# Performance work log

Hardware: AMD Instinct MI355X
Metric: run time of the kernel (lower is better)

Reference implementation:

```python
import jax, jax.numpy as jnp
import numpy as np

MEM_SIZE = 1_000_000
DIM = 128
BS = 256
K = 1024
TEMP = 0.07
MOM_V = 0.5
MOM_A = 0.5


def _l2norm(x, axis=-1, eps=1e-12):
    n = jnp.sqrt(jnp.sum(x * x, axis=axis, keepdims=True))
    return x / jnp.maximum(n, eps)


def setup_inputs() -> dict:
    key = jax.random.key(0)
    k1, k2, k3, k4, k5, k6 = jax.random.split(key, 6)
    video_emb = jax.random.normal(k1, (BS, DIM), dtype=jnp.float32)
    audio_emb = jax.random.normal(k2, (BS, DIM), dtype=jnp.float32)
    y = jax.random.randint(k3, (BS,), 0, MEM_SIZE, dtype=jnp.int32)
    # alias method draws over memory_size-1 items (before shifting past y)
    neg_idx = jax.random.randint(k4, (BS, K), 0, MEM_SIZE - 1, dtype=jnp.int32)
    view1_mem = _l2norm(jax.random.normal(k5, (MEM_SIZE, DIM), dtype=jnp.float32))
    view2_mem = _l2norm(jax.random.normal(k6, (MEM_SIZE, DIM), dtype=jnp.float32))
    return {
        "video_emb": video_emb,
        "audio_emb": audio_emb,
        "y": y,
        "neg_idx": neg_idx,
        "view1_mem": view1_mem,
        "view2_mem": view2_mem,
    }


def reference(video_emb, audio_emb, y, neg_idx, view1_mem, view2_mem):
    v = _l2norm(video_emb, axis=1)   # [bs, dim]
    a = _l2norm(audio_emb, axis=1)   # [bs, dim]

    # shift negative indices past the positive index y (as in sample_negatives)
    idx = neg_idx + (neg_idx >= y[:, None]).astype(neg_idx.dtype)  # [bs, K]

    # gather positives / negatives from memory banks
    v_pos = view1_mem[y]           # [bs, dim]
    a_pos = view2_mem[y]           # [bs, dim]
    v_neg = view1_mem[idx]         # [bs, K, dim]
    a_neg = view2_mem[idx]         # [bs, K, dim]

    # xModal scores (wModal=False)
    v2a_pos = jnp.einsum("bd,bd->b", a_pos, v)[:, None] / TEMP    # [bs, 1]
    v2a_neg = jnp.einsum("bkd,bd->bk", a_neg, v) / TEMP           # [bs, K]
    a2v_pos = jnp.einsum("bd,bd->b", v_pos, a)[:, None] / TEMP    # [bs, 1]
    a2v_neg = jnp.einsum("bkd,bd->bk", v_neg, a) / TEMP           # [bs, K]

    scores = jnp.stack(
        [jnp.concatenate([v2a_pos, v2a_neg], axis=1),
         jnp.concatenate([a2v_pos, a2v_neg], axis=1)],
        axis=0,
    )  # [2, bs, K+1]

    # momentum scatter update of memory banks (no_grad in original)
    new1 = _l2norm(MOM_V * v_pos + (1.0 - MOM_V) * v, axis=1)
    new2 = _l2norm(MOM_A * a_pos + (1.0 - MOM_A) * a, axis=1)
    view1_new = view1_mem.at[y].set(new1)
    view2_new = view2_mem.at[y].set(new2)

    return scores, view1_new, view2_new
```

## Files before the change

### kernel.cpp

```cpp
#include <hip/hip_runtime.h>

#define MEM_SIZE 1000000
#define DIM 128
#define BS 256
#define K 1024
#define NSC (K + 1)
#define OVFCAP 32768

constexpr float INV_TEMP = 1.0f / 0.07f;
constexpr float MOM = 0.5f;

#define NB 2048
#define BT 128
#define NWAVES (NB * BT / 64)

typedef float fx4 __attribute__((ext_vector_type(4)));

#define QTAB_OFF 0
#define CNT_OFF  262144
#define SLOT_OFF 4456448
#define OVFC_OFF 12845056
#define OVF_OFF  12845312
#define WS_NEED  13107456

__device__ __forceinline__ float wave_reduce_sum(float v) {
    #pragma unroll
    for (int off = 32; off > 0; off >>= 1)
        v += __shfl_xor(v, off, 64);
    return v;
}

__global__ __launch_bounds__(BT) void setup_kernel(
    const float* __restrict__ video, const float* __restrict__ audio,
    float* __restrict__ qtab, int* __restrict__ counts,
    int* __restrict__ slots_i, int* __restrict__ ovf_cnt) {
    const int bid = blockIdx.x;
    const int t = threadIdx.x;
    const int tid = bid * BT + t;
    if (bid < 256) {
        const int u = bid * 2 + (t >> 6);
        const int lane = t & 63;
        const int b = u & (BS - 1);
        const float* src = (u < BS) ? video : audio;
        const float2 e = reinterpret_cast<const float2*>(src + b * DIM)[lane];
        const float ss = wave_reduce_sum(e.x * e.x + e.y * e.y);
        const float inv = 1.0f / fmaxf(sqrtf(ss), 1e-12f);
        reinterpret_cast<float2*>(qtab + u * DIM)[lane] =
            make_float2(e.x * inv, e.y * inv);
    }
    for (int i = tid; i < MEM_SIZE; i += NB * BT) counts[i] = 0;
    for (int i = tid; i < 2 * MEM_SIZE; i += NB * BT) slots_i[i] = -1;
    if (tid == 0) *ovf_cnt = 0;
}

__global__ void build_kernel(const int* __restrict__ y,
                             const int* __restrict__ neg,
                             int* __restrict__ counts,
                             int* __restrict__ slots_i,
                             int* __restrict__ ovf_cnt,
                             int2* __restrict__ ovf) {
    const int E = blockIdx.x * blockDim.x + threadIdx.x;
    int b, j, row;
    if (E < BS * K) {
        b = E >> 10;
        const int jj = E & 1023;
        j = jj + 1;
        const int ni = neg[b * K + jj];
        const int yb = y[b];
        row = ni + (ni >= yb ? 1 : 0);
    } else {
        b = E - BS * K;
        if (b >= BS) return;
        j = 0;
        row = y[b];
    }
    const int key = (b << 11) | j;
    const int old = atomicAdd(&counts[row], 1);
    if (old < 2) {
        slots_i[row * 2 + old] = key;
    } else {
        const int p = atomicAdd(ovf_cnt, 1);
        if (p < OVFCAP) ovf[p] = make_int2(row, key);
    }
}

__global__ __launch_bounds__(BT, 4) void main_kernel(
    const float* __restrict__ view1, const float* __restrict__ view2,
    const float* __restrict__ qtab, const int2* __restrict__ slots,
    float* __restrict__ scores,
    fx4* __restrict__ out1, fx4* __restrict__ out2) {
    const int tid = blockIdx.x * BT + threadIdx.x;
    const int wid = tid >> 6;
    const int lane = tid & 63;
    const int half = lane >> 5;
    const int hl = lane & 31;
    const fx4* s1 = reinterpret_cast<const fx4*>(view1);
    const fx4* s2 = reinterpret_cast<const fx4*>(view2);
    const fx4* qt4 = reinterpret_cast<const fx4*>(qtab);

    const long long n4 = (long long)MEM_SIZE * DIM / 4;
    for (long long wbase = (long long)wid * 64; wbase < n4;
         wbase += (long long)NWAVES * 64) {
        const long long i = wbase + lane;
        const fx4 a = s1[i];
        const fx4 c = s2[i];
        const int row = (int)(wbase >> 5) + half;
        const int2 sl = slots[row];
        __builtin_nontemporal_store(a, &out1[i]);
        __builtin_nontemporal_store(c, &out2[i]);

        if (__any(sl.x >= 0)) {
            #pragma unroll
            for (int t = 0; t < 2; ++t) {
                const int key = (t == 0) ? sl.x : sl.y;
                if (key >= 0) {
                    const int b = key >> 11;
                    const int j = key & 2047;
                    const fx4 q0 = qt4[b * 32 + hl];
                    const fx4 q1 = qt4[(256 + b) * 32 + hl];
                    float d0 = q0.x * c.x + q0.y * c.y + q0.z * c.z + q0.w * c.w;
                    float d1 = q1.x * a.x + q1.y * a.y + q1.z * a.z + q1.w * a.w;
                    #pragma unroll
                    for (int off = 16; off > 0; off >>= 1) {
                        d0 += __shfl_xor(d0, off, 64);
                        d1 += __shfl_xor(d1, off, 64);
                    }
                    if (hl == 0) {
                        scores[b * NSC + j] = d0 * INV_TEMP;
                        scores[(256 + b) * NSC + j] = d1 * INV_TEMP;
                    }
                }
            }
        }
    }
}

__global__ void tail_kernel(const float* __restrict__ video,
                            const float* __restrict__ audio,
                            const int* __restrict__ y,
                            const float* __restrict__ view1,
                            const float* __restrict__ view2,
                            const float* __restrict__ qtab,
                            const int* __restrict__ ovf_cnt,
                            const int2* __restrict__ ovf,
                            float* __restrict__ scores,
                            float* __restrict__ out1,
                            float* __restrict__ out2) {
    const int blk = blockIdx.x;
    const int lane = threadIdx.x;
    if (blk < 512) {
        const int bank = blk >> 8;
        const int b = blk & (BS - 1);
        const int row = y[b];
        for (int b2 = b + 1; b2 < BS; ++b2)
            if (y[b2] == row) return;
        const float* emb = (bank == 0) ? video : audio;
        const float2 e = reinterpret_cast<const float2*>(emb + b * DIM)[lane];
        const float ss = wave_reduce_sum(e.x * e.x + e.y * e.y);
        const float inv = 1.0f / fmaxf(sqrtf(ss), 1e-12f);
        const float* mem = (bank == 0) ? view1 : view2;
        const float2 xp =
            reinterpret_cast<const float2*>(mem + (size_t)row * DIM)[lane];
        float2 nv = make_float2(MOM * xp.x + (1.0f - MOM) * e.x * inv,
                                MOM * xp.y + (1.0f - MOM) * e.y * inv);
        const float ss2 = wave_reduce_sum(nv.x * nv.x + nv.y * nv.y);
        const float inv2 = 1.0f / fmaxf(sqrtf(ss2), 1e-12f);
        float* out = (bank == 0) ? out1 : out2;
        reinterpret_cast<float2*>(out + (size_t)row * DIM)[lane] =
            make_float2(nv.x * inv2, nv.y * inv2);
    } else {
        int n = *ovf_cnt;
        if (n > OVFCAP) n = OVFCAP;
        const float2* m1 = reinterpret_cast<const float2*>(view1);
        const float2* m2 = reinterpret_cast<const float2*>(view2);
        const float2* qt2 = reinterpret_cast<const float2*>(qtab);
        for (int e = blk - 512; e < n; e += 128) {
            const int2 rk = ovf[e];
            const int row = rk.x, key = rk.y;
            const int b = key >> 11, j = key & 2047;
            const float2 xa = m1[(size_t)row * 64 + lane];
            const float2 xc = m2[(size_t)row * 64 + lane];
            const float2 q0 = qt2[(size_t)b * 64 + lane];
            const float2 q1 = qt2[(size_t)(256 + b) * 64 + lane];
            float d0 = xc.x * q0.x + xc.y * q0.y;
            float d1 = xa.x * q1.x + xa.y * q1.y;
            #pragma unroll
            for (int off = 32; off > 0; off >>= 1) {
                d0 += __shfl_xor(d0, off, 64);
                d1 += __shfl_xor(d1, off, 64);
            }
            if (lane == 0) {
                scores[b * NSC + j] = d0 * INV_TEMP;
                scores[(256 + b) * NSC + j] = d1 * INV_TEMP;
            }
        }
    }
}

__global__ __launch_bounds__(256) void fb_fused(
    const float* __restrict__ video, const float* __restrict__ audio,
    const int* __restrict__ y, const int* __restrict__ neg,
    const float* __restrict__ view1, const float* __restrict__ view2,
    float* __restrict__ scores,
    fx4* __restrict__ out1, fx4* __restrict__ out2) {
    const int bid = blockIdx.x;
    const int tid = threadIdx.x;
    if ((bid & 3) == 0) {
        const int bm = bid >> 2;
        const int m = bm >> 8;
        const int b = bm & (BS - 1);
        const int lane = tid & 63;
        const int wv = tid >> 6;
        const int yb = y[b];
        const float* emb = (m == 0) ? video : audio;
        const float2 e = reinterpret_cast<const float2*>(emb + b * DIM)[lane];
        const float ss = wave_reduce_sum(e.x * e.x + e.y * e.y);
        const float inv = 1.0f / fmaxf(sqrtf(ss), 1e-12f);
        const float vx = e.x * inv, vy = e.y * inv;
        const float2* mem2 =
            reinterpret_cast<const float2*>((m == 0) ? view2 : view1);
        float* srow = scores + (size_t)bm * NSC;
        const int* nb = neg + b * K;
        const int chunk = (NSC + 3) / 4;
        const int j0 = wv * chunk;
        const int j1 = min(NSC, j0 + chunk);
        for (int j = j0; j < j1; ++j) {
            int r0;
            if (j == 0) r0 = yb;
            else { const int ni = nb[j - 1]; r0 = ni + (ni >= yb ? 1 : 0); }
            const float2 x0 = mem2[(size_t)r0 * 64 + lane];
            const float s0 = wave_reduce_sum(x0.x * vx + x0.y * vy);
            if (lane == 0) srow[j] = s0 * INV_TEMP;
        }
    } else {
        const long long n4 = (long long)MEM_SIZE * DIM / 4;
        const int cb = bid - (bid >> 2) - 1;
        const fx4* s1 = reinterpret_cast<const fx4*>(view1);
        const fx4* s2 = reinterpret_cast<const fx4*>(view2);
        long long i = (long long)cb * blockDim.x + tid;
        const long long stride = (long long)1536 * blockDim.x;
        for (; i < n4; i += stride) {
            const fx4 a = __builtin_nontemporal_load(&s1[i]);
            const fx4 c = __builtin_nontemporal_load(&s2[i]);
            __builtin_nontemporal_store(a, &out1[i]);
            __builtin_nontemporal_store(c, &out2[i]);
        }
    }
}

__global__ void fb_scatter(const float* __restrict__ video,
                           const float* __restrict__ audio,
                           const int* __restrict__ y,
                           const float* __restrict__ view1,
                           const float* __restrict__ view2,
                           float* __restrict__ out1,
                           float* __restrict__ out2) {
    const int blk = blockIdx.x;
    const int lane = threadIdx.x;
    const int bank = blk >> 8;
    const int b = blk & (BS - 1);
    const int row = y[b];
    for (int b2 = b + 1; b2 < BS; ++b2)
        if (y[b2] == row) return;
    const float* emb = (bank == 0) ? video : audio;
    const float2 e = reinterpret_cast<const float2*>(emb + b * DIM)[lane];
    const float ss = wave_reduce_sum(e.x * e.x + e.y * e.y);
    const float inv = 1.0f / fmaxf(sqrtf(ss), 1e-12f);
    const float* mem = (bank == 0) ? view1 : view2;
    const float2 xp =
        reinterpret_cast<const float2*>(mem + (size_t)row * DIM)[lane];
    float2 nv = make_float2(MOM * xp.x + (1.0f - MOM) * e.x * inv,
                            MOM * xp.y + (1.0f - MOM) * e.y * inv);
    const float ss2 = wave_reduce_sum(nv.x * nv.x + nv.y * nv.y);
    const float inv2 = 1.0f / fmaxf(sqrtf(ss2), 1e-12f);
    float* out = (bank == 0) ? out1 : out2;
    reinterpret_cast<float2*>(out + (size_t)row * DIM)[lane] =
        make_float2(nv.x * inv2, nv.y * inv2);
}

extern "C" void kernel_launch(void* const* d_in, const int* in_sizes, int n_in,
                              void* d_out, int out_size, void* d_ws, size_t ws_size,
                              hipStream_t stream) {
    const float* video = (const float*)d_in[0];
    const float* audio = (const float*)d_in[1];
    const int* y       = (const int*)d_in[2];
    const int* neg     = (const int*)d_in[3];
    const float* v1    = (const float*)d_in[4];
    const float* v2    = (const float*)d_in[5];

    float* out    = (float*)d_out;
    float* scores = out;
    float* out1   = out + 2 * BS * NSC;
    float* out2   = out1 + (size_t)MEM_SIZE * DIM;

    if (ws_size < (size_t)WS_NEED) {
        fb_fused<<<2048, 256, 0, stream>>>(video, audio, y, neg, v1, v2,
                                           scores, (fx4*)out1, (fx4*)out2);
        fb_scatter<<<512, 64, 0, stream>>>(video, audio, y, v1, v2, out1, out2);
        return;
    }

    char* ws = (char*)d_ws;
    float* qtab  = (float*)(ws + QTAB_OFF);
    int* counts  = (int*)(ws + CNT_OFF);
    int* slots_i = (int*)(ws + SLOT_OFF);
    int2* slots  = (int2*)(ws + SLOT_OFF);
    int* ovf_cnt = (int*)(ws + OVFC_OFF);
    int2* ovf    = (int2*)(ws + OVF_OFF);

    setup_kernel<<<NB, BT, 0, stream>>>(video, audio, qtab, counts,
                                        slots_i, ovf_cnt);
    build_kernel<<<1025, 256, 0, stream>>>(y, neg, counts, slots_i,
                                           ovf_cnt, ovf);
    main_kernel<<<NB, BT, 0, stream>>>(v1, v2, qtab, slots,
                                       scores, (fx4*)out1, (fx4*)out2);
    tail_kernel<<<640, 64, 0, stream>>>(video, audio, y, v1, v2, qtab,
                                        ovf_cnt, ovf, scores, out1, out2);
}
```

Before: 468.7 us.

## Replace count array with CAS slot claims, prefetch slots, widen overflow tail

The separate per-row counts array goes away. Build now claims the two slots per row with atomicCAS on -1 sentinels, which removes a 4 MB zero-fill and one atomic per entry. The main streaming loop prefetches the next iteration's slot pair so that load overlaps the copy. The tail kernel gets more blocks for overflow entries. The slot array is padded so the prefetch past the end stays in bounds, at the cost of extra CAS traffic when a row is contended.

After: 449.3 us. 4.1% less time.

```diff
diff --git a/kernel.cpp b/kernel.cpp
--- a/kernel.cpp
+++ b/kernel.cpp
@@ -6,6 +6,7 @@
 #define K 1024
 #define NSC (K + 1)
 #define OVFCAP 32768
+#define SLOT_ENT 1008704
 
 constexpr float INV_TEMP = 1.0f / 0.07f;
 constexpr float MOM = 0.5f;
@@ -13,15 +14,15 @@
 #define NB 2048
 #define BT 128
 #define NWAVES (NB * BT / 64)
+#define STEP ((long long)NWAVES * 64)
 
 typedef float fx4 __attribute__((ext_vector_type(4)));
 
 #define QTAB_OFF 0
-#define CNT_OFF  262144
-#define SLOT_OFF 4456448
-#define OVFC_OFF 12845056
-#define OVF_OFF  12845312
-#define WS_NEED  13107456
+#define SLOT_OFF 262144
+#define OVFC_OFF 8331776
+#define OVF_OFF  8332032
+#define WS_NEED  8594176
 
 __device__ __forceinline__ float wave_reduce_sum(float v) {
     #pragma unroll
@@ -32,8 +33,8 @@
 
 __global__ __launch_bounds__(BT) void setup_kernel(
     const float* __restrict__ video, const float* __restrict__ audio,
-    float* __restrict__ qtab, int* __restrict__ counts,
-    int* __restrict__ slots_i, int* __restrict__ ovf_cnt) {
+    float* __restrict__ qtab, int* __restrict__ slots_i,
+    int* __restrict__ ovf_cnt) {
     const int bid = blockIdx.x;
     const int t = threadIdx.x;
     const int tid = bid * BT + t;
@@ -48,14 +49,12 @@
         reinterpret_cast<float2*>(qtab + u * DIM)[lane] =
             make_float2(e.x * inv, e.y * inv);
     }
-    for (int i = tid; i < MEM_SIZE; i += NB * BT) counts[i] = 0;
-    for (int i = tid; i < 2 * MEM_SIZE; i += NB * BT) slots_i[i] = -1;
+    for (int i = tid; i < 2 * SLOT_ENT; i += NB * BT) slots_i[i] = -1;
     if (tid == 0) *ovf_cnt = 0;
 }
 
 __global__ void build_kernel(const int* __restrict__ y,
                              const int* __restrict__ neg,
-                             int* __restrict__ counts,
                              int* __restrict__ slots_i,
                              int* __restrict__ ovf_cnt,
                              int2* __restrict__ ovf) {
@@ -75,12 +74,11 @@
         row = y[b];
     }
     const int key = (b << 11) | j;
-    const int old = atomicAdd(&counts[row], 1);
-    if (old < 2) {
-        slots_i[row * 2 + old] = key;
-    } else {
-        const int p = atomicAdd(ovf_cnt, 1);
-        if (p < OVFCAP) ovf[p] = make_int2(row, key);
+    if (atomicCAS(&slots_i[row * 2], -1, key) != -1) {
+        if (atomicCAS(&slots_i[row * 2 + 1], -1, key) != -1) {
+            const int p = atomicAdd(ovf_cnt, 1);
+            if (p < OVFCAP) ovf[p] = make_int2(row, key);
+        }
     }
 }
 
@@ -99,13 +97,13 @@
     const fx4* qt4 = reinterpret_cast<const fx4*>(qtab);
 
     const long long n4 = (long long)MEM_SIZE * DIM / 4;
-    for (long long wbase = (long long)wid * 64; wbase < n4;
-         wbase += (long long)NWAVES * 64) {
+    long long wbase = (long long)wid * 64;
+    int2 sl = slots[wid * 2 + half];
+    for (; wbase < n4; wbase += STEP) {
         const long long i = wbase + lane;
         const fx4 a = s1[i];
         const fx4 c = s2[i];
-        const int row = (int)(wbase >> 5) + half;
-        const int2 sl = slots[row];
+        const int2 sl_next = slots[(int)((wbase + STEP) >> 5) + half];
         __builtin_nontemporal_store(a, &out1[i]);
         __builtin_nontemporal_store(c, &out2[i]);
 
@@ -132,6 +130,7 @@
                 }
             }
         }
+        sl = sl_next;
     }
 }
 
@@ -174,7 +173,7 @@
         const float2* m1 = reinterpret_cast<const float2*>(view1);
         const float2* m2 = reinterpret_cast<const float2*>(view2);
         const float2* qt2 = reinterpret_cast<const float2*>(qtab);
-        for (int e = blk - 512; e < n; e += 128) {
+        for (int e = blk - 512; e < n; e += 512) {
             const int2 rk = ovf[e];
             const int row = rk.x, key = rk.y;
             const int b = key >> 11, j = key & 2047;
@@ -302,18 +301,15 @@
 
     char* ws = (char*)d_ws;
     float* qtab  = (float*)(ws + QTAB_OFF);
-    int* counts  = (int*)(ws + CNT_OFF);
     int* slots_i = (int*)(ws + SLOT_OFF);
     int2* slots  = (int2*)(ws + SLOT_OFF);
     int* ovf_cnt = (int*)(ws + OVFC_OFF);
     int2* ovf    = (int2*)(ws + OVF_OFF);
 
-    setup_kernel<<<NB, BT, 0, stream>>>(video, audio, qtab, counts,
-                                        slots_i, ovf_cnt);
-    build_kernel<<<1025, 256, 0, stream>>>(y, neg, counts, slots_i,
-                                           ovf_cnt, ovf);
+    setup_kernel<<<NB, BT, 0, stream>>>(video, audio, qtab, slots_i, ovf_cnt);
+    build_kernel<<<1025, 256, 0, stream>>>(y, neg, slots_i, ovf_cnt, ovf);
     main_kernel<<<NB, BT, 0, stream>>>(v1, v2, qtab, slots,
                                        scores, (fx4*)out1, (fx4*)out2);
-    tail_kernel<<<640, 64, 0, stream>>>(video, audio, y, v1, v2, qtab,
-                                        ovf_cnt, ovf, scores, out1, out2);
-}
+    tail_kernel<<<1024, 64, 0, stream>>>(video, audio, y, v1, v2, qtab,
+                                         ovf_cnt, ovf, scores, out1, out2);
+}
```
